# Kernel optimization log

Measured on AMD Instinct MI355X. Metric: run time of the kernel, lower is better.

## Reference

```python
import jax, jax.numpy as jnp
import numpy as np

D = 1024      # model dim
H = 16        # num heads
HD = D // H   # head dim = 64
B, N, M = 4, 4096, 256
EPS = 1e-12   # torch F.normalize eps


def setup_inputs() -> dict:
    key = jax.random.key(0)
    ks = jax.random.split(key, 11)
    s = 0.02  # weight init scale
    W = lambda k: jax.random.normal(k, (D, D), jnp.float32) * s
    return {
        "x": jax.random.normal(ks[0], (B, N, D), jnp.float32),
        "c": jax.random.normal(ks[1], (B, M, D), jnp.float32),
        "Wq_x": W(ks[2]), "Wk_x": W(ks[3]), "Wv_x": W(ks[4]),
        "Wq_c": W(ks[5]), "Wk_c": W(ks[6]), "Wv_c": W(ks[7]),
        "Wo_x": W(ks[8]), "Wo_c": W(ks[9]),
        "norm_const": 0.5 * jnp.ones((1, H, 1, 1), jnp.float32),
    }


def _heads(t):
    # (B, S, D) -> (B, H, S, HD)
    b, s, _ = t.shape
    return t.reshape(b, s, H, HD).transpose(0, 2, 1, 3)


def _l2norm(t):
    n = jnp.linalg.norm(t, axis=-1, keepdims=True)
    return t / jnp.maximum(n, EPS)


def reference(x, c, Wq_x, Wk_x, Wv_x, Wq_c, Wk_c, Wv_c, Wo_x, Wo_c, norm_const):
    b, n, d = x.shape
    m = c.shape[1]
    # fused QKV projections for each stream (Linear, no bias: y = t @ W^T)
    qx = _l2norm(_heads(x @ Wq_x.T))   # (B,H,N,HD), cosine-normalized
    kx = _l2norm(_heads(x @ Wk_x.T))
    vx = _heads(x @ Wv_x.T)
    qc = _l2norm(_heads(c @ Wq_c.T))   # (B,H,M,HD)
    kc = _l2norm(_heads(c @ Wk_c.T))
    vc = _heads(c @ Wv_c.T)
    # concat streams along the sequence axis
    q = jnp.concatenate([qx, qc], axis=2)   # (B,H,N+M,HD)
    k = jnp.concatenate([kx, kc], axis=2)
    v = jnp.concatenate([vx, vc], axis=2)
    n_tot = n + m
    # cosine (linear) attention, non-causal: values scaled by N^sigmoid(norm_const)
    v = v / (jnp.float32(n_tot) ** jax.nn.sigmoid(norm_const))
    kv = jnp.einsum("bhnd,bhne->bhde", k, v)         # (B,H,HD,HD)
    attn = jnp.einsum("bhnd,bhde->bhne", q, kv)      # (B,H,N+M,HD)
    # split streams, merge heads, output projections
    attn_x = attn[:, :, :n].transpose(0, 2, 1, 3).reshape(b, n, H * HD)
    attn_c = attn[:, :, n:].transpose(0, 2, 1, 3).reshape(b, m, H * HD)
    out_x = attn_x @ Wo_x.T
    out_c = attn_c @ Wo_c.T
    return out_x, out_c
```

## Files before the change

### kernel.cpp

```cpp
#include <hip/hip_runtime.h>
#include <cstdint>

typedef unsigned int u32;
typedef unsigned short u16;
typedef float fx4 __attribute__((ext_vector_type(4)));
typedef __bf16 bfx8 __attribute__((ext_vector_type(8)));

__device__ __forceinline__ u16 f2bf(float f) {
  u32 u = __builtin_bit_cast(u32, f);
  u32 r = (u + 0x7fffu + ((u >> 16) & 1u)) >> 16;
  return (u16)r;
}
__device__ __forceinline__ float bf2f(u16 v) {
  return __builtin_bit_cast(float, (u32)v << 16);
}
__device__ __forceinline__ void async_copy16(const void* g, void* l) {
  auto gp = reinterpret_cast<__attribute__((address_space(1))) void*>((uintptr_t)g);
  auto lp = reinterpret_cast<__attribute__((address_space(3))) void*>((uintptr_t)l);
  __builtin_amdgcn_global_load_lds(gp, lp, 16, 0, 0);
}

__global__ __launch_bounds__(256) void cvt_all(
    const float* __restrict__ x, const float* __restrict__ c,
    const float* __restrict__ w0, const float* __restrict__ w1,
    const float* __restrict__ w2, const float* __restrict__ w3,
    const float* __restrict__ w4, const float* __restrict__ w5,
    const float* __restrict__ w6, const float* __restrict__ w7,
    u16* __restrict__ xb, u16* __restrict__ cb, u16* __restrict__ wb) {
  const int i = blockIdx.x * 256 + threadIdx.x;
  const float* src;
  u16* dst;
  size_t off;
  if (i < 4194304) {
    src = x; dst = xb; off = (size_t)i;
  } else if (i < 4456448) {
    src = c; dst = cb; off = (size_t)(i - 4194304);
  } else {
    const int r = i - 4456448;
    const int wsel = r >> 18;
    off = (size_t)(r & 262143);
    switch (wsel) {
      case 0: src = w0; break; case 1: src = w1; break;
      case 2: src = w2; break; case 3: src = w3; break;
      case 4: src = w4; break; case 5: src = w5; break;
      case 6: src = w6; break; default: src = w7; break;
    }
    dst = wb + (size_t)wsel * 1048576;
  }
  const fx4 v = *(const fx4*)(src + off * 4);
  uint2 o;
  o.x = (u32)f2bf(v[0]) | ((u32)f2bf(v[1]) << 16);
  o.y = (u32)f2bf(v[2]) | ((u32)f2bf(v[3]) << 16);
  *(uint2*)(dst + off * 4) = o;
}

#define GC_DSB(BUF, KS)                                                        \
  _Pragma("unroll") for (int i_ = 0; i_ < 4; ++i_) bfr[i_] =                   \
      *(const bfx8*)(lds + (BUF) + 16384 + (KS) * 8192 + wc * 2048 + i_ * 512 + aLane);
#define GC_DSA(BUF, KS, H)                                                     \
  _Pragma("unroll") for (int i_ = 0; i_ < 4; ++i_) af[i_] =                    \
      *(const bfx8*)(lds + (BUF) + (KS) * 8192 + wr * 4096 + (H) * 2048 + i_ * 512 + aLane);
#define GC_STA(REG, KCOL)                                                      \
  async_copy16(Aop + aOff0 + (KCOL), lds + (REG) + dst0);                      \
  async_copy16(Aop + aOff1 + (KCOL), lds + (REG) + dst1);
#define GC_STB(REG, KCOL)                                                      \
  async_copy16(Bop + bOff0 + (KCOL), lds + (REG) + dst0);                      \
  async_copy16(Bop + bOff1 + (KCOL), lds + (REG) + dst1);
#define GC_MFMA(H)                                                             \
  __builtin_amdgcn_s_setprio(1);                                               \
  _Pragma("unroll") for (int mi_ = 0; mi_ < 4; ++mi_)                          \
  _Pragma("unroll") for (int ni_ = 0; ni_ < 4; ++ni_)                          \
      acc[(H) * 4 + mi_][ni_] = __builtin_amdgcn_mfma_f32_16x16x32_bf16(       \
          af[mi_], bfr[ni_], acc[(H) * 4 + mi_][ni_], 0, 0, 0);                \
  __builtin_amdgcn_s_setprio(0);
#define GC_MID()                                                               \
  __builtin_amdgcn_s_barrier();                                                \
  asm volatile("s_waitcnt lgkmcnt(0)" ::: "memory");                           \
  __builtin_amdgcn_sched_barrier(0);
#define GC_END()                                                               \
  __builtin_amdgcn_s_barrier();                                                \
  __builtin_amdgcn_sched_barrier(0);

__device__ __forceinline__ void gemm256_core(
    const u16* __restrict__ Aop, const u16* __restrict__ Bop,
    long rowBase, long colBase, u16* lds, fx4 (&acc)[8][4]) {
  const int t = threadIdx.x;
  const int lane = t & 63;
  const int lr = lane & 15;
  const int quad = lane >> 4;
  const int w = t >> 6;
  const int wr = w >> 2;
  const int wc = w & 3;
  const int phys = (((lr & 1) << 2) | quad) ^ ((lr >> 1) & 7);
  const int aLane = ((lr >> 1) << 6) + (phys << 3);

  int aOff0, aOff1, bOff0, bOff1, dst0, dst1;
  {
    const int c0 = t;
    const int R0 = c0 >> 3;
    const int lg0 = (c0 & 7) ^ (R0 & 7);
    const int m0_ = 2 * R0 + (lg0 >> 2);
    const int g0 = lg0 & 3;
    aOff0 = (int)(rowBase + m0_) * 1024 + g0 * 8;
    bOff0 = (int)(colBase + m0_) * 1024 + g0 * 8;
    dst0 = c0 * 8;
    const int c1 = t + 512;
    const int R1 = c1 >> 3;
    const int lg1 = (c1 & 7) ^ (R1 & 7);
    const int m1_ = 2 * R1 + (lg1 >> 2);
    const int g1 = lg1 & 3;
    aOff1 = (int)(rowBase + m1_) * 1024 + g1 * 8;
    bOff1 = (int)(colBase + m1_) * 1024 + g1 * 8;
    dst1 = c1 * 8;
  }

  GC_STA(0, 0) GC_STB(16384, 0) GC_STA(8192, 32) GC_STB(24576, 32)
  GC_STA(32768, 64) GC_STB(49152, 64)
  asm volatile("s_waitcnt vmcnt(8)" ::: "memory");
  __builtin_amdgcn_s_barrier();
  __builtin_amdgcn_sched_barrier(0);

  bfx8 bfr[4];
  for (int it = 0; it < 8; ++it) {
    const bool lastI = (it == 7);
    const int k1 = (2 * it + 1) * 64 + 32;
    const int k2 = (2 * it + 2) * 64;
    const int k3 = k2 + 32;
    const int k4 = (2 * it + 3) * 64;
    { bfx8 af[4];
      GC_DSB(0, 0) GC_DSA(0, 0, 0)
      GC_STA(40960, k1)
      GC_MID() GC_MFMA(0) GC_END() }
    { bfx8 af[4];
      GC_DSA(0, 0, 1)
      GC_STB(57344, k1)
      GC_MID() GC_MFMA(1)
      asm volatile("s_waitcnt vmcnt(8)" ::: "memory");
      GC_END() }
    { bfx8 af[4];
      GC_DSB(0, 1) GC_DSA(0, 1, 0)
      if (!lastI) { GC_STA(0, k2) }
      GC_MID() GC_MFMA(0) GC_END() }
    { bfx8 af[4];
      GC_DSA(0, 1, 1)
      if (!lastI) { GC_STB(16384, k2) }
      GC_MID() GC_MFMA(1)
      if (lastI) { asm volatile("s_waitcnt vmcnt(4)" ::: "memory"); }
      else       { asm volatile("s_waitcnt vmcnt(8)" ::: "memory"); }
      GC_END() }
    { bfx8 af[4];
      GC_DSB(32768, 0) GC_DSA(32768, 0, 0)
      if (!lastI) { GC_STA(8192, k3) }
      GC_MID() GC_MFMA(0) GC_END() }
    { bfx8 af[4];
      GC_DSA(32768, 0, 1)
      if (!lastI) { GC_STB(24576, k3) }
      GC_MID() GC_MFMA(1)
      if (lastI) { asm volatile("s_waitcnt vmcnt(0)" ::: "memory"); }
      else       { asm volatile("s_waitcnt vmcnt(8)" ::: "memory"); }
      GC_END() }
    { bfx8 af[4];
      GC_DSB(32768, 1) GC_DSA(32768, 1, 0)
      if (!lastI) { GC_STA(32768, k4) }
      GC_MID() GC_MFMA(0) GC_END() }
    { bfx8 af[4];
      GC_DSA(32768, 1, 1)
      if (!lastI) { GC_STB(49152, k4) }
      GC_MID() GC_MFMA(1)
      if (!lastI) { asm volatile("s_waitcnt vmcnt(8)" ::: "memory"); }
      GC_END() }
  }
}

__global__ __launch_bounds__(512, 2) void proj_fused(
    const u16* __restrict__ Xb, const u16* __restrict__ Cb, const u16* __restrict__ Wb,
    u16* __restrict__ Qx, u16* __restrict__ Qc,
    u16* __restrict__ Kt, u16* __restrict__ Vt,
    const float* __restrict__ nc) {
  extern __shared__ __align__(16) u16 lds[];
  const int bid = (int)(blockIdx.y * 12 + blockIdx.x);
  const int u = (bid & 7) * 102 + (bid >> 3);
  const int yy = u / 12;
  const int xx = u - yy * 12;
  const bool isC = yy >= 64;
  const u16* A = isC ? Cb : Xb;
  const u16* Bw = Wb + (isC ? 3145728 : 0);
  const long rowBase = (long)(isC ? yy - 64 : yy) * 256;
  const long colBase = (long)xx * 256;

  fx4 acc[8][4] = {};
  gemm256_core(A, Bw, rowBase, colBase, lds, acc);

  const int t = threadIdx.x;
  const int lane = t & 63;
  const int lr = lane & 15;
  const int quad = lane >> 4;
  const int w = t >> 6;
  const int wr = w >> 2;
  const int wc = w & 3;
  const long wRowBase = rowBase + wr * 128;

  const long col0 = colBase + wc * 64;
  const int col64 = (int)(col0 >> 6);
  const int sel = col64 >> 4;
  const int h = col64 & 15;
  const int lcolBase = (int)(col0 & 1023);

  if (sel == 0) {
    u16* dst = isC ? Qc : Qx;
#pragma unroll
    for (int mi = 0; mi < 8; ++mi) {
      float ss[4] = {0.f, 0.f, 0.f, 0.f};
#pragma unroll
      for (int ni = 0; ni < 4; ++ni)
#pragma unroll
        for (int r = 0; r < 4; ++r) ss[r] += acc[mi][ni][r] * acc[mi][ni][r];
#pragma unroll
      for (int off = 1; off < 16; off <<= 1)
#pragma unroll
        for (int r = 0; r < 4; ++r) ss[r] += __shfl_xor(ss[r], off, 64);
      float sc[4];
#pragma unroll
      for (int r = 0; r < 4; ++r) sc[r] = 1.f / fmaxf(sqrtf(ss[r]), 1e-12f);
#pragma unroll
      for (int ni = 0; ni < 4; ++ni) {
        const long col = lcolBase + ni * 16 + lr;
#pragma unroll
        for (int r = 0; r < 4; ++r) {
          const long row = wRowBase + mi * 16 + quad * 4 + r;
          dst[row * 1024 + col] = f2bf(acc[mi][ni][r] * sc[r]);
        }
      }
    }
  } else {
    __syncthreads();
    u16* LT = lds + w * 8192;
    u16* T = (sel == 1) ? Kt : Vt;
    int b, nglob0;
    if (!isC) { b = (int)(wRowBase >> 12); nglob0 = (int)(wRowBase & 4095); }
    else      { b = (int)(wRowBase >> 8);  nglob0 = 4096 + (int)(wRowBase & 255); }
    u16* Tw = T + (size_t)(b * 16 + h) * 64 * 4352;
    const float vs = __expf(-8.3783908f / (1.f + __expf(-nc[h])));

#pragma unroll
    for (int mi = 0; mi < 8; ++mi) {
      float sc[4];
      if (sel == 1) {
        float ss[4] = {0.f, 0.f, 0.f, 0.f};
#pragma unroll
        for (int ni = 0; ni < 4; ++ni)
#pragma unroll
          for (int r = 0; r < 4; ++r) ss[r] += acc[mi][ni][r] * acc[mi][ni][r];
#pragma unroll
      for (int off = 1; off < 16; off <<= 1)
#pragma unroll
          for (int r = 0; r < 4; ++r) ss[r] += __shfl_xor(ss[r], off, 64);
#pragma unroll
        for (int r = 0; r < 4; ++r) sc[r] = 1.f / fmaxf(sqrtf(ss[r]), 1e-12f);
      } else {
#pragma unroll
        for (int r = 0; r < 4; ++r) sc[r] = vs;
      }
      const int g = mi * 2 + (quad >> 1);
      const int sub = (quad & 1) * 4;
#pragma unroll
      for (int ni = 0; ni < 4; ++ni) {
        const int d = ni * 16 + lr;
        uint2 o;
        o.x = (u32)f2bf(acc[mi][ni][0] * sc[0]) | ((u32)f2bf(acc[mi][ni][1] * sc[1]) << 16);
        o.y = (u32)f2bf(acc[mi][ni][2] * sc[2]) | ((u32)f2bf(acc[mi][ni][3] * sc[3]) << 16);
        *(uint2*)&LT[d * 128 + ((g ^ (d & 15)) << 3) + sub] = o;
      }
    }
    __syncthreads();
    const int d = lane;
    u16* drow = Tw + (size_t)d * 4352 + nglob0;
#pragma unroll
    for (int j = 0; j < 16; ++j) {
      const uint4 qv = *(const uint4*)&LT[d * 128 + ((j ^ (d & 15)) << 3)];
      *(uint4*)&drow[j * 8] = qv;
    }
  }
}

__global__ __launch_bounds__(256) void kv_mfma(
    const u16* __restrict__ Kt, const u16* __restrict__ Vt, float* __restrict__ kvp) {
  __shared__ __align__(16) u16 TT[4][2][4096];
  const int bh = blockIdx.x;
  const int t = threadIdx.x;
  const int w = t >> 6;
  const int lane = t & 63;
  const int lr = lane & 15;
  const int quad = lane >> 4;
  const u16* Ksrc = Kt + (size_t)bh * 64 * 4352;
  const u16* Vsrc = Vt + (size_t)bh * 64 * 4352;
  const int row8 = lane >> 3;
  const int gst = lane & 7;
  fx4 acc[4][4] = {};

  const int kbase = (blockIdx.y * 4 + w) * 64;
#pragma unroll
  for (int i = 0; i < 8; ++i) {
    const int row = i * 8 + row8;
    const int col = ((gst ^ (row & 7)) << 3);
    const size_t go = (size_t)row * 4352 + kbase + col;
    async_copy16(Ksrc + go, &TT[w][0][i * 512 + lane * 8]);
    async_copy16(Vsrc + go, &TT[w][1][i * 512 + lane * 8]);
  }
  __syncthreads();
#pragma unroll
  for (int ks = 0; ks < 2; ++ks) {
    bfx8 af[4], bfr[4];
    const int g = ((ks * 4 + quad) ^ (lr & 7)) << 3;
#pragma unroll
    for (int i = 0; i < 4; ++i) af[i] = *(const bfx8*)&TT[w][0][(i * 16 + lr) * 64 + g];
#pragma unroll
    for (int i = 0; i < 4; ++i) bfr[i] = *(const bfx8*)&TT[w][1][(i * 16 + lr) * 64 + g];
#pragma unroll
    for (int mi = 0; mi < 4; ++mi)
#pragma unroll
      for (int ni = 0; ni < 4; ++ni)
        acc[mi][ni] =
            __builtin_amdgcn_mfma_f32_16x16x32_bf16(af[mi], bfr[ni], acc[mi][ni], 0, 0, 0);
  }
  __syncthreads();
  float* red = (float*)&TT[0][0][0];
  float* my = red + w * 4096;
#pragma unroll
  for (int mi = 0; mi < 4; ++mi)
#pragma unroll
    for (int ni = 0; ni < 4; ++ni) {
      const int e = ni * 16 + lr;
      const int dg = mi * 4 + quad;
      *(fx4*)&my[e * 64 + ((dg ^ (e & 15)) << 2)] = acc[mi][ni];
    }
  __syncthreads();
  float* outp = kvp + ((size_t)blockIdx.y * 64 + bh) * 4096;
#pragma unroll
  for (int j = 0; j < 4; ++j) {
    const int L = t * 16 + j * 4;
    const int e = L >> 6;
    const int dg = (L >> 2) & 15;
    const int addr = e * 64 + ((dg ^ (e & 15)) << 2);
    fx4 sv = *(const fx4*)&red[addr];
    sv += *(const fx4*)&red[4096 + addr];
    sv += *(const fx4*)&red[8192 + addr];
    sv += *(const fx4*)&red[12288 + addr];
    *(fx4*)&outp[L] = sv;
  }
}

__global__ __launch_bounds__(256) void kv_reduce(
    const float* __restrict__ kvp, float* __restrict__ kvb) {
  const int o = blockIdx.x * 256 + threadIdx.x;
  const int bh = o >> 10;
  const int idx = (o & 1023) * 4;
  fx4 s = {0.f, 0.f, 0.f, 0.f};
#pragma unroll
  for (int y = 0; y < 17; ++y)
    s += *(const fx4*)&kvp[((size_t)y * 64 + bh) * 4096 + idx];
  *(fx4*)&kvb[(size_t)bh * 4096 + idx] = s;
}

__global__ __launch_bounds__(256) void weff_build(
    const u16* __restrict__ WoX, const u16* __restrict__ WoC,
    const float* __restrict__ kvb, u16* __restrict__ WeffX, u16* __restrict__ WeffC) {
  const int ot = blockIdx.x;
  const int bh = blockIdx.y;
  const int b = bh >> 4, h = bh & 15;
  const u16* Wo = blockIdx.z ? WoC : WoX;
  u16* outp = (blockIdx.z ? WeffC : WeffX) + (size_t)b * 1048576;

  __shared__ __align__(16) float kvT[64 * 64];
  __shared__ __align__(16) float WoT[64 * 64];
  const int t = threadIdx.x;
#pragma unroll
  for (int j = 0; j < 4; ++j) {
    const int idx = (t + 256 * j) * 4;
    *(fx4*)&kvT[idx] = *(const fx4*)&kvb[(size_t)bh * 4096 + idx];
  }
#pragma unroll
  for (int j = 0; j < 2; ++j) {
    const int u = t + 256 * j;
    const int row = u >> 3;
    const int e0 = (u & 7) * 8;
    const uint4 q = *(const uint4*)&Wo[(size_t)(ot * 64 + row) * 1024 + h * 64 + e0];
    WoT[(e0 + 0) * 64 + row] = bf2f((u16)(q.x & 0xffff));
    WoT[(e0 + 1) * 64 + row] = bf2f((u16)(q.x >> 16));
    WoT[(e0 + 2) * 64 + row] = bf2f((u16)(q.y & 0xffff));
    WoT[(e0 + 3) * 64 + row] = bf2f((u16)(q.y >> 16));
    WoT[(e0 + 4) * 64 + row] = bf2f((u16)(q.z & 0xffff));
    WoT[(e0 + 5) * 64 + row] = bf2f((u16)(q.z >> 16));
    WoT[(e0 + 6) * 64 + row] = bf2f((u16)(q.w & 0xffff));
    WoT[(e0 + 7) * 64 + row] = bf2f((u16)(q.w >> 16));
  }
  __syncthreads();
  const int ob = (t >> 4) * 4;
  const int db = (t & 15) * 4;
  float acc[4][4] = {};
#pragma unroll 4
  for (int e = 0; e < 64; ++e) {
    const fx4 wv = *(const fx4*)&WoT[e * 64 + ob];
    const fx4 kvv = *(const fx4*)&kvT[e * 64 + db];
#pragma unroll
    for (int i = 0; i < 4; ++i)
#pragma unroll
      for (int j = 0; j < 4; ++j)
        acc[i][j] += wv[i] * kvv[j];
  }
#pragma unroll
  for (int i = 0; i < 4; ++i)
#pragma unroll
    for (int j = 0; j < 4; ++j)
      outp[(size_t)(ot * 64 + ob + i) * 1024 + h * 64 + db + j] = f2bf(acc[i][j]);
}

__global__ __launch_bounds__(512, 2) void out_fused(
    const u16* __restrict__ Qx, const u16* __restrict__ Qc,
    const u16* __restrict__ Wex, const u16* __restrict__ Wec,
    float* __restrict__ out) {
  extern __shared__ __align__(16) u16 lds[];
  const int bid = (int)(blockIdx.y * 4 + blockIdx.x);
  const int u = (bid & 7) * 34 + (bid >> 3);
  const int yt = u >> 2;
  const int xx = u & 3;
  const int b = yt / 17;
  const int l = yt - b * 17;
  const bool isC = (l == 16);
  const u16* A;
  const u16* Bw;
  float* C;
  long rowBase;
  if (!isC) {
    A = Qx + (size_t)b * 4194304;
    Bw = Wex + (size_t)b * 1048576;
    C = out + (size_t)b * 4194304;
    rowBase = (long)l * 256;
  } else {
    A = Qc + (size_t)b * 262144;
    Bw = Wec + (size_t)b * 1048576;
    C = out + 16777216 + (size_t)b * 262144;
    rowBase = 0;
  }
  const long colBase = (long)xx * 256;

  fx4 acc[8][4] = {};
  gemm256_core(A, Bw, rowBase, colBase, lds, acc);

  const int t = threadIdx.x;
  const int lane = t & 63;
  const int lr = lane & 15;
  const int quad = lane >> 4;
  const int w = t >> 6;
  const int wr = w >> 2;
  const int wc = w & 3;
#pragma unroll
  for (int mi = 0; mi < 8; ++mi)
#pragma unroll
    for (int ni = 0; ni < 4; ++ni) {
      const long col = colBase + wc * 64 + ni * 16 + lr;
#pragma unroll
      for (int r = 0; r < 4; ++r) {
        const long row = rowBase + wr * 128 + mi * 16 + quad * 4 + r;
        C[row * 1024 + col] = acc[mi][ni][r];
      }
    }
}

extern "C" void kernel_launch(void* const* d_in, const int* in_sizes, int n_in,
                              void* d_out, int out_size, void* d_ws, size_t ws_size,
                              hipStream_t stream) {
  (void)in_sizes; (void)n_in; (void)out_size; (void)ws_size;
  const float* x = (const float*)d_in[0];
  const float* c = (const float*)d_in[1];
  const float* nc = (const float*)d_in[10];
  float* out = (float*)d_out;
  char* ws = (char*)d_ws;

  static bool attr_done = false;
  if (!attr_done) {
    hipFuncSetAttribute((const void*)proj_fused,
                        hipFuncAttributeMaxDynamicSharedMemorySize, 131072);
    hipFuncSetAttribute((const void*)out_fused,
                        hipFuncAttributeMaxDynamicSharedMemorySize, 131072);
    attr_done = true;
  }

  u16* Xb = (u16*)(ws + 0);
  u16* Cb = (u16*)(ws + 33554432);
  u16* Wb = (u16*)(ws + 35651584);
  u16* Qx = (u16*)(ws + 52428800);
  u16* Qc = (u16*)(ws + 85983232);
  u16* Kt = (u16*)(ws + 88080384);
  u16* Vt = (u16*)(ws + 123731968);
  float* kvb = (float*)(ws + 159383552);
  u16* Weffx = (u16*)(ws + 160432128);
  u16* Weffc = (u16*)(ws + 168820736);
  float* kvp = (float*)(ws + 0);

  cvt_all<<<25600, 256, 0, stream>>>(
      x, c, (const float*)d_in[2], (const float*)d_in[3], (const float*)d_in[4],
      (const float*)d_in[5], (const float*)d_in[6], (const float*)d_in[7],
      (const float*)d_in[8], (const float*)d_in[9], Xb, Cb, Wb);

  proj_fused<<<dim3(12, 68), 512, 131072, stream>>>(Xb, Cb, Wb, Qx, Qc, Kt, Vt, nc);
  kv_mfma<<<dim3(64, 17), 256, 0, stream>>>(Kt, Vt, kvp);
  kv_reduce<<<256, 256, 0, stream>>>(kvp, kvb);
  weff_build<<<dim3(16, 64, 2), 256, 0, stream>>>(Wb + 6 * 1048576, Wb + 7 * 1048576,
                                                  kvb, Weffx, Weffc);
  out_fused<<<dim3(4, 68), 512, 131072, stream>>>(Qx, Qc, Weffx, Weffc, out);
}
```

Baseline: 399.6 us.

## Replace 4-stage GEMM pipeline with simple double buffer and halve LDS

The GEMM core's hand-scheduled multi-stage prefetch ring (128 KB LDS) becomes a two-buffer loop over 32-wide K tiles, with one load and one full vmcnt wait per step. The K/V transpose epilogue is split into two halves so it fits the smaller per-wave scratch. Dynamic LDS for both GEMM kernels drops to 64 KB, which could allow more resident blocks per CU. The trade-off is a shallower prefetch, with a full memory wait and two barriers every K step, so global latency is less hidden.

```diff
diff --git a/kernel.cpp b/kernel.cpp
--- a/kernel.cpp
+++ b/kernel.cpp
@@ -54,32 +54,18 @@
   *(uint2*)(dst + off * 4) = o;
 }
 
-#define GC_DSB(BUF, KS)                                                        \
+#define GC2_DS()                                                               \
   _Pragma("unroll") for (int i_ = 0; i_ < 4; ++i_) bfr[i_] =                   \
-      *(const bfx8*)(lds + (BUF) + 16384 + (KS) * 8192 + wc * 2048 + i_ * 512 + aLane);
-#define GC_DSA(BUF, KS, H)                                                     \
-  _Pragma("unroll") for (int i_ = 0; i_ < 4; ++i_) af[i_] =                    \
-      *(const bfx8*)(lds + (BUF) + (KS) * 8192 + wr * 4096 + (H) * 2048 + i_ * 512 + aLane);
-#define GC_STA(REG, KCOL)                                                      \
-  async_copy16(Aop + aOff0 + (KCOL), lds + (REG) + dst0);                      \
-  async_copy16(Aop + aOff1 + (KCOL), lds + (REG) + dst1);
-#define GC_STB(REG, KCOL)                                                      \
-  async_copy16(Bop + bOff0 + (KCOL), lds + (REG) + dst0);                      \
-  async_copy16(Bop + bOff1 + (KCOL), lds + (REG) + dst1);
-#define GC_MFMA(H)                                                             \
-  __builtin_amdgcn_s_setprio(1);                                               \
-  _Pragma("unroll") for (int mi_ = 0; mi_ < 4; ++mi_)                          \
-  _Pragma("unroll") for (int ni_ = 0; ni_ < 4; ++ni_)                          \
-      acc[(H) * 4 + mi_][ni_] = __builtin_amdgcn_mfma_f32_16x16x32_bf16(       \
-          af[mi_], bfr[ni_], acc[(H) * 4 + mi_][ni_], 0, 0, 0);                \
-  __builtin_amdgcn_s_setprio(0);
-#define GC_MID()                                                               \
-  __builtin_amdgcn_s_barrier();                                                \
-  asm volatile("s_waitcnt lgkmcnt(0)" ::: "memory");                           \
-  __builtin_amdgcn_sched_barrier(0);
-#define GC_END()                                                               \
-  __builtin_amdgcn_s_barrier();                                                \
-  __builtin_amdgcn_sched_barrier(0);
+      *(const bfx8*)(lds + bufo + 8192 + wc * 2048 + i_ * 512 + aLane);        \
+  _Pragma("unroll") for (int i_ = 0; i_ < 4; ++i_) af0[i_] =                   \
+      *(const bfx8*)(lds + bufo + wr * 4096 + i_ * 512 + aLane);               \
+  _Pragma("unroll") for (int i_ = 0; i_ < 4; ++i_) af1[i_] =                   \
+      *(const bfx8*)(lds + bufo + wr * 4096 + 2048 + i_ * 512 + aLane);
+#define GC2_ST(BUF, KT)                                                        \
+  async_copy16(Aop + aOff0 + (KT) * 32, lds + (BUF) + dst0);                   \
+  async_copy16(Aop + aOff1 + (KT) * 32, lds + (BUF) + dst1);                   \
+  async_copy16(Bop + bOff0 + (KT) * 32, lds + (BUF) + 8192 + dst0);            \
+  async_copy16(Bop + bOff1 + (KT) * 32, lds + (BUF) + 8192 + dst1);
 
 __device__ __forceinline__ void gemm256_core(
     const u16* __restrict__ Aop, const u16* __restrict__ Bop,
@@ -114,61 +100,38 @@
     dst1 = c1 * 8;
   }
 
-  GC_STA(0, 0) GC_STB(16384, 0) GC_STA(8192, 32) GC_STB(24576, 32)
-  GC_STA(32768, 64) GC_STB(49152, 64)
-  asm volatile("s_waitcnt vmcnt(8)" ::: "memory");
+  GC2_ST(0, 0)
+  asm volatile("s_waitcnt vmcnt(0)" ::: "memory");
   __builtin_amdgcn_s_barrier();
   __builtin_amdgcn_sched_barrier(0);
 
-  bfx8 bfr[4];
-  for (int it = 0; it < 8; ++it) {
-    const bool lastI = (it == 7);
-    const int k1 = (2 * it + 1) * 64 + 32;
-    const int k2 = (2 * it + 2) * 64;
-    const int k3 = k2 + 32;
-    const int k4 = (2 * it + 3) * 64;
-    { bfx8 af[4];
-      GC_DSB(0, 0) GC_DSA(0, 0, 0)
-      GC_STA(40960, k1)
-      GC_MID() GC_MFMA(0) GC_END() }
-    { bfx8 af[4];
-      GC_DSA(0, 0, 1)
-      GC_STB(57344, k1)
-      GC_MID() GC_MFMA(1)
-      asm volatile("s_waitcnt vmcnt(8)" ::: "memory");
-      GC_END() }
-    { bfx8 af[4];
-      GC_DSB(0, 1) GC_DSA(0, 1, 0)
-      if (!lastI) { GC_STA(0, k2) }
-      GC_MID() GC_MFMA(0) GC_END() }
-    { bfx8 af[4];
-      GC_DSA(0, 1, 1)
-      if (!lastI) { GC_STB(16384, k2) }
-      GC_MID() GC_MFMA(1)
-      if (lastI) { asm volatile("s_waitcnt vmcnt(4)" ::: "memory"); }
-      else       { asm volatile("s_waitcnt vmcnt(8)" ::: "memory"); }
-      GC_END() }
-    { bfx8 af[4];
-      GC_DSB(32768, 0) GC_DSA(32768, 0, 0)
-      if (!lastI) { GC_STA(8192, k3) }
-      GC_MID() GC_MFMA(0) GC_END() }
-    { bfx8 af[4];
-      GC_DSA(32768, 0, 1)
-      if (!lastI) { GC_STB(24576, k3) }
-      GC_MID() GC_MFMA(1)
-      if (lastI) { asm volatile("s_waitcnt vmcnt(0)" ::: "memory"); }
-      else       { asm volatile("s_waitcnt vmcnt(8)" ::: "memory"); }
-      GC_END() }
-    { bfx8 af[4];
-      GC_DSB(32768, 1) GC_DSA(32768, 1, 0)
-      if (!lastI) { GC_STA(32768, k4) }
-      GC_MID() GC_MFMA(0) GC_END() }
-    { bfx8 af[4];
-      GC_DSA(32768, 1, 1)
-      if (!lastI) { GC_STB(49152, k4) }
-      GC_MID() GC_MFMA(1)
-      if (!lastI) { asm volatile("s_waitcnt vmcnt(8)" ::: "memory"); }
-      GC_END() }
+  for (int tt = 0; tt < 32; ++tt) {
+    const int bufo = (tt & 1) << 14;
+    const int nbuf = ((tt + 1) & 1) << 14;
+    bfx8 af0[4], af1[4], bfr[4];
+    if (tt < 31) { GC2_ST(nbuf, tt + 1) }
+    GC2_DS()
+    __builtin_amdgcn_s_barrier();
+    asm volatile("s_waitcnt lgkmcnt(0)" ::: "memory");
+    __builtin_amdgcn_sched_barrier(0);
+    __builtin_amdgcn_s_setprio(1);
+#pragma unroll
+    for (int mi = 0; mi < 4; ++mi)
+#pragma unroll
+      for (int ni = 0; ni < 4; ++ni)
+        acc[mi][ni] =
+            __builtin_amdgcn_mfma_f32_16x16x32_bf16(af0[mi], bfr[ni], acc[mi][ni], 0, 0, 0);
+#pragma unroll
+    for (int mi = 0; mi < 4; ++mi)
+#pragma unroll
+      for (int ni = 0; ni < 4; ++ni)
+        acc[4 + mi][ni] =
+            __builtin_amdgcn_mfma_f32_16x16x32_bf16(af1[mi], bfr[ni], acc[4 + mi][ni], 0, 0, 0);
+    __builtin_amdgcn_s_setprio(0);
+    __builtin_amdgcn_sched_barrier(0);
+    if (tt < 31) { asm volatile("s_waitcnt vmcnt(0)" ::: "memory"); }
+    __builtin_amdgcn_s_barrier();
+    __builtin_amdgcn_sched_barrier(0);
   }
 }
 
@@ -233,52 +196,56 @@
       }
     }
   } else {
-    __syncthreads();
-    u16* LT = lds + w * 8192;
+    u16* LT = lds + w * 4096;
     u16* T = (sel == 1) ? Kt : Vt;
     int b, nglob0;
     if (!isC) { b = (int)(wRowBase >> 12); nglob0 = (int)(wRowBase & 4095); }
     else      { b = (int)(wRowBase >> 8);  nglob0 = 4096 + (int)(wRowBase & 255); }
     u16* Tw = T + (size_t)(b * 16 + h) * 64 * 4352;
     const float vs = __expf(-8.3783908f / (1.f + __expf(-nc[h])));
-
-#pragma unroll
-    for (int mi = 0; mi < 8; ++mi) {
-      float sc[4];
-      if (sel == 1) {
-        float ss[4] = {0.f, 0.f, 0.f, 0.f};
-#pragma unroll
-        for (int ni = 0; ni < 4; ++ni)
-#pragma unroll
-          for (int r = 0; r < 4; ++r) ss[r] += acc[mi][ni][r] * acc[mi][ni][r];
-#pragma unroll
-      for (int off = 1; off < 16; off <<= 1)
-#pragma unroll
-          for (int r = 0; r < 4; ++r) ss[r] += __shfl_xor(ss[r], off, 64);
-#pragma unroll
-        for (int r = 0; r < 4; ++r) sc[r] = 1.f / fmaxf(sqrtf(ss[r]), 1e-12f);
-      } else {
-#pragma unroll
-        for (int r = 0; r < 4; ++r) sc[r] = vs;
-      }
-      const int g = mi * 2 + (quad >> 1);
-      const int sub = (quad & 1) * 4;
-#pragma unroll
-      for (int ni = 0; ni < 4; ++ni) {
-        const int d = ni * 16 + lr;
-        uint2 o;
-        o.x = (u32)f2bf(acc[mi][ni][0] * sc[0]) | ((u32)f2bf(acc[mi][ni][1] * sc[1]) << 16);
-        o.y = (u32)f2bf(acc[mi][ni][2] * sc[2]) | ((u32)f2bf(acc[mi][ni][3] * sc[3]) << 16);
-        *(uint2*)&LT[d * 128 + ((g ^ (d & 15)) << 3) + sub] = o;
-      }
-    }
-    __syncthreads();
     const int d = lane;
     u16* drow = Tw + (size_t)d * 4352 + nglob0;
-#pragma unroll
-    for (int j = 0; j < 16; ++j) {
-      const uint4 qv = *(const uint4*)&LT[d * 128 + ((j ^ (d & 15)) << 3)];
-      *(uint4*)&drow[j * 8] = qv;
+
+#pragma unroll
+    for (int half = 0; half < 2; ++half) {
+      __syncthreads();
+#pragma unroll
+      for (int mi2 = 0; mi2 < 4; ++mi2) {
+        const int mi = half * 4 + mi2;
+        float sc[4];
+        if (sel == 1) {
+          float ss[4] = {0.f, 0.f, 0.f, 0.f};
+#pragma unroll
+          for (int ni = 0; ni < 4; ++ni)
+#pragma unroll
+            for (int r = 0; r < 4; ++r) ss[r] += acc[mi][ni][r] * acc[mi][ni][r];
+#pragma unroll
+          for (int off = 1; off < 16; off <<= 1)
+#pragma unroll
+            for (int r = 0; r < 4; ++r) ss[r] += __shfl_xor(ss[r], off, 64);
+#pragma unroll
+          for (int r = 0; r < 4; ++r) sc[r] = 1.f / fmaxf(sqrtf(ss[r]), 1e-12f);
+        } else {
+#pragma unroll
+          for (int r = 0; r < 4; ++r) sc[r] = vs;
+        }
+        const int g = mi2 * 2 + (quad >> 1);
+        const int sub = (quad & 1) * 4;
+#pragma unroll
+        for (int ni = 0; ni < 4; ++ni) {
+          const int dd = ni * 16 + lr;
+          uint2 o;
+          o.x = (u32)f2bf(acc[mi][ni][0] * sc[0]) | ((u32)f2bf(acc[mi][ni][1] * sc[1]) << 16);
+          o.y = (u32)f2bf(acc[mi][ni][2] * sc[2]) | ((u32)f2bf(acc[mi][ni][3] * sc[3]) << 16);
+          *(uint2*)&LT[dd * 64 + ((g ^ (dd & 7)) << 3) + sub] = o;
+        }
+      }
+      __syncthreads();
+#pragma unroll
+      for (int j = 0; j < 8; ++j) {
+        const uint4 qv = *(const uint4*)&LT[d * 64 + ((j ^ (d & 7)) << 3)];
+        *(uint4*)&drow[half * 64 + j * 8] = qv;
+      }
     }
   }
 }
@@ -480,9 +447,9 @@
   static bool attr_done = false;
   if (!attr_done) {
     hipFuncSetAttribute((const void*)proj_fused,
-                        hipFuncAttributeMaxDynamicSharedMemorySize, 131072);
+                        hipFuncAttributeMaxDynamicSharedMemorySize, 65536);
     hipFuncSetAttribute((const void*)out_fused,
-                        hipFuncAttributeMaxDynamicSharedMemorySize, 131072);
+                        hipFuncAttributeMaxDynamicSharedMemorySize, 65536);
     attr_done = true;
   }
 
@@ -503,10 +470,10 @@
       (const float*)d_in[5], (const float*)d_in[6], (const float*)d_in[7],
       (const float*)d_in[8], (const float*)d_in[9], Xb, Cb, Wb);
 
-  proj_fused<<<dim3(12, 68), 512, 131072, stream>>>(Xb, Cb, Wb, Qx, Qc, Kt, Vt, nc);
+  proj_fused<<<dim3(12, 68), 512, 65536, stream>>>(Xb, Cb, Wb, Qx, Qc, Kt, Vt, nc);
   kv_mfma<<<dim3(64, 17), 256, 0, stream>>>(Kt, Vt, kvp);
   kv_reduce<<<256, 256, 0, stream>>>(kvp, kvb);
   weff_build<<<dim3(16, 64, 2), 256, 0, stream>>>(Wb + 6 * 1048576, Wb + 7 * 1048576,
                                                   kvb, Weffx, Weffc);
-  out_fused<<<dim3(4, 68), 512, 131072, stream>>>(Qx, Qc, Weffx, Weffc, out);
-}
+  out_fused<<<dim3(4, 68), 512, 65536, stream>>>(Qx, Qc, Weffx, Weffc, out);
+}
```

Result: slower. 412.7 us (+3.3%).
